# Performance work log

Measured on AMD Instinct MI355X. Metric: run time of the kernel, lower is better.

The kernel has to match this reference:

```python
import jax, jax.numpy as jnp
import numpy as np
import math

TANH_CLIP = 10.0
NEG_INF = -100000000.0

def setup_inputs() -> dict:
    key = jax.random.key(0)
    k1, k2, k3, k4, k5 = jax.random.split(key, 5)
    B, Nq, Nk, D = 64, 1024, 1024, 256
    scale = 1.0 / math.sqrt(D)  # ~xavier-ish scale for weights
    return {
        "q": jax.random.normal(k1, (B, Nq, D), dtype=jnp.float32),
        "k": jax.random.normal(k2, (B, Nk, D), dtype=jnp.float32),
        "w_query": jax.random.normal(k3, (D, D), dtype=jnp.float32) * scale,
        "w_key": jax.random.normal(k4, (D, D), dtype=jnp.float32) * scale,
        "mask": jax.random.randint(k5, (B, Nq, Nk), 0, 2, dtype=jnp.int32),
    }

def reference(q, k, w_query, w_key, mask):
    D = q.shape[-1]
    norm = 1.0 / math.sqrt(D)  # key_dim == embedding_dim
    Q = jnp.einsum("bqd,de->bqe", q, w_query)  # [B,Nq,D]
    K = jnp.einsum("bkd,de->bke", k, w_key)    # [B,Nk,D]
    U = norm * jnp.einsum("bqe,bke->bqk", Q, K)
    U = TANH_CLIP * jnp.tanh(U)
    U = jnp.where(mask == 1, NEG_INF, U)
    return jax.nn.log_softmax(U, axis=-1)
```

## Files before the change

### kernel.cpp

```cpp
#include <hip/hip_runtime.h>
#include <hip/hip_bf16.h>
#include <stdint.h>

#define NEG_INF -100000000.0f

typedef __attribute__((ext_vector_type(8))) short bf16x8;
typedef __attribute__((ext_vector_type(4))) float f32x4;
typedef __attribute__((ext_vector_type(4))) int i32x4;

#define LGKM_BAR()                                                \
    do {                                                          \
        asm volatile("s_waitcnt lgkmcnt(0)" ::: "memory");        \
        __builtin_amdgcn_s_barrier();                             \
        __builtin_amdgcn_sched_barrier(0);                        \
    } while (0)

static __device__ __forceinline__ short f2bf(float x) {
    unsigned u = __float_as_uint(x);
    u = u + 0x7FFFu + ((u >> 16) & 1u);
    return (short)(u >> 16);
}

__global__ void wtrans_kernel(const float* __restrict__ wq, const float* __restrict__ wk,
                              short* __restrict__ wtq, short* __restrict__ wtk) {
    __shared__ float tile[32][33];
    const float* w = blockIdx.z ? wk : wq;
    short* wt = blockIdx.z ? wtk : wtq;
    float scale = blockIdx.z ? 1.0f : 0.0625f;
    int tx = threadIdx.x, ty = threadIdx.y;
    int c0 = blockIdx.x * 32;
    int k0 = blockIdx.y * 32;
#pragma unroll
    for (int i = 0; i < 4; i++)
        tile[ty + i * 8][tx] = w[(k0 + ty + i * 8) * 256 + c0 + tx];
    __syncthreads();
#pragma unroll
    for (int i = 0; i < 4; i++)
        wt[(c0 + ty + i * 8) * 256 + k0 + tx] = f2bf(tile[tx][ty + i * 8] * scale);
}

__global__ __launch_bounds__(512, 4)
void proj_kernel(const float* __restrict__ qin, const float* __restrict__ kin,
                 const short* __restrict__ wtq, const short* __restrict__ wtk,
                 short* __restrict__ Qb, short* __restrict__ Kb,
                 const int* __restrict__ mask, unsigned* __restrict__ pmask) {
    if (blockIdx.y == 2) {
        int t = threadIdx.x;
        size_t row = (size_t)blockIdx.x * 64 + (t >> 3);
        int seg8 = t & 7;
        const int* mrow = mask + row * 1024;
#pragma unroll
        for (int jj = 0; jj < 4; jj++) {
            int j = seg8 + jj * 8;
            unsigned v = 0;
#pragma unroll
            for (int i = 0; i < 8; i++) {
                i32x4 x = __builtin_nontemporal_load(
                    reinterpret_cast<const i32x4*>(mrow + j * 4 + i * 128));
                unsigned nib = (unsigned)(x.x | (x.y << 1) | (x.z << 2) | (x.w << 3));
                v |= nib << (i * 4);
            }
            pmask[row * 32 + j] = v;
        }
        return;
    }

    const float* x  = blockIdx.y ? kin : qin;
    const short* wt = blockIdx.y ? wtk : wtq;
    short* outp     = blockIdx.y ? Kb  : Qb;

    __shared__ __align__(16) short sbuf[64 * 296];
    short* xlds = sbuf;
    short* wlds = sbuf + 2048;

    int t = threadIdx.x;
    int lane = t & 63, w = t >> 6;
    int l15 = lane & 15, g = lane >> 4;
    int rowbase = blockIdx.x * 64;

    f32x4 zero = {0.f, 0.f, 0.f, 0.f};
    f32x4 acc[4][2];
#pragma unroll
    for (int m = 0; m < 4; m++)
#pragma unroll
        for (int n = 0; n < 2; n++) acc[m][n] = zero;

    for (int dc = 0; dc < 8; dc++) {
        __syncthreads();
        {
            int row = t >> 3, seg = t & 7;
            f32x4 v = __builtin_nontemporal_load(
                reinterpret_cast<const f32x4*>(x + (size_t)(rowbase + row) * 256 + dc * 32 + seg * 4));
            short4 bb;
            bb.x = f2bf(v.x); bb.y = f2bf(v.y); bb.z = f2bf(v.z); bb.w = f2bf(v.w);
            *reinterpret_cast<short4*>(&xlds[row * 32 + seg * 4]) = bb;
        }
#pragma unroll
        for (int i = 0; i < 2; i++) {
            int idx = i * 512 + t;
            int c = idx >> 2, seg = idx & 3;
            int4 v = *reinterpret_cast<const int4*>(wt + c * 256 + dc * 32 + seg * 8);
            *reinterpret_cast<int4*>(&wlds[idx * 8]) = v;
        }
        __syncthreads();

        bf16x8 a[4], bfr[2];
#pragma unroll
        for (int m = 0; m < 4; m++)
            a[m] = *reinterpret_cast<const bf16x8*>(&xlds[(m * 16 + l15) * 32 + g * 8]);
#pragma unroll
        for (int n = 0; n < 2; n++) {
            int c = w * 32 + n * 16 + l15;
            bfr[n] = *reinterpret_cast<const bf16x8*>(&wlds[c * 32 + g * 8]);
        }
#pragma unroll
        for (int m = 0; m < 4; m++)
#pragma unroll
            for (int n = 0; n < 2; n++)
                acc[m][n] = __builtin_amdgcn_mfma_f32_16x16x32_bf16(a[m], bfr[n], acc[m][n], 0, 0, 0);
    }

    __syncthreads();
#pragma unroll
    for (int m = 0; m < 4; m++)
#pragma unroll
        for (int n = 0; n < 2; n++) {
            int col = w * 32 + n * 16 + l15;
#pragma unroll
            for (int r = 0; r < 4; r++)
                sbuf[(m * 16 + g * 4 + r) * 296 + col] = f2bf(acc[m][n][r]);
        }
    __syncthreads();

    int b8 = rowbase >> 10;
    int rloc = rowbase & 1023;
#pragma unroll
    for (int o = 0; o < 4; o++) {
        int gu = o * 512 + t;
        int dc = gu >> 8;
        int rem = gu & 255;
        int row = rem >> 2, kseg = rem & 3;
        int4 v = *reinterpret_cast<const int4*>(&sbuf[row * 296 + dc * 32 + kseg * 8]);
        size_t idx = (((size_t)b8 * 8 + dc) * 1024 + rloc + row) * 32 + kseg * 8;
        *reinterpret_cast<int4*>(outp + idx) = v;
    }
}

__global__ __launch_bounds__(512, 4)
void attn_kernel(const short* __restrict__ Qs, const short* __restrict__ Ks,
                 const unsigned* __restrict__ pmask, float* __restrict__ out) {
    const int RS = 1028;
    __shared__ __align__(16) float ulds[16 * RS];

    int t = threadIdx.x;
    int lane = t & 63, w = t >> 6;
    int l15 = lane & 15, g = lane >> 4;

    int bid = blockIdx.x;
    int wg = (bid & 7) * 256 + (bid >> 3);
    int b = wg >> 5;
    int brow = (wg & 31) * 32;

    const unsigned* pm = pmask + ((size_t)b * 1024 + brow) * 32;
    unsigned mbits0 = pm[t];
    unsigned mbits1 = pm[512 + t];

    const short* qb = Qs + (size_t)b * 8 * 1024 * 32;
    const short* kb = Ks + (size_t)b * 8 * 1024 * 32;

    f32x4 zero = {0.f, 0.f, 0.f, 0.f};
    f32x4 acc[2][8];
#pragma unroll
    for (int m = 0; m < 2; m++)
#pragma unroll
        for (int n = 0; n < 8; n++) acc[m][n] = zero;

    for (int dc = 0; dc < 8; dc++) {
        const short* qc = qb + (size_t)dc * 1024 * 32;
        const short* kc = kb + (size_t)dc * 1024 * 32;
        bf16x8 a0 = *reinterpret_cast<const bf16x8*>(qc + (brow + l15) * 32 + g * 8);
        bf16x8 a1 = *reinterpret_cast<const bf16x8*>(qc + (brow + 16 + l15) * 32 + g * 8);
#pragma unroll
        for (int n = 0; n < 8; n++) {
            bf16x8 bf = *reinterpret_cast<const bf16x8*>(kc + (w * 128 + n * 16 + l15) * 32 + g * 8);
            acc[0][n] = __builtin_amdgcn_mfma_f32_16x16x32_bf16(a0, bf, acc[0][n], 0, 0, 0);
            acc[1][n] = __builtin_amdgcn_mfma_f32_16x16x32_bf16(a1, bf, acc[1][n], 0, 0, 0);
        }
    }

    int row = t >> 5;
    int j = t & 31;
    float* urow = ulds + row * RS;

#pragma unroll
    for (int m = 0; m < 2; m++) {
        LGKM_BAR();
#pragma unroll
        for (int n = 0; n < 8; n++)
#pragma unroll
            for (int r = 0; r < 4; r++)
                ulds[(g * 4 + r) * RS + w * 128 + n * 16 + l15] = acc[m][n][r];
        LGKM_BAR();

        unsigned bits = m ? mbits1 : mbits0;

        float psum = 0.f;
#pragma unroll
        for (int i = 0; i < 8; i++) {
            int col = j * 4 + i * 128;
            float4 u4 = *reinterpret_cast<const float4*>(urow + col);
            float uv[4] = {u4.x, u4.y, u4.z, u4.w};
            float uc[4];
#pragma unroll
            for (int c = 0; c < 4; c++) {
                float e2 = __expf(2.0f * uv[c]);
                float tc = 10.0f - 20.0f / (e2 + 1.0f);
                bool msk = (bits >> (i * 4 + c)) & 1;
                uc[c] = msk ? NEG_INF : tc;
                psum += msk ? 0.0f : __expf(tc);
            }
            float4 s = {uc[0], uc[1], uc[2], uc[3]};
            *reinterpret_cast<float4*>(urow + col) = s;
        }
        psum += __shfl_xor(psum, 1);
        psum += __shfl_xor(psum, 2);
        psum += __shfl_xor(psum, 4);
        psum += __shfl_xor(psum, 8);
        psum += __shfl_xor(psum, 16);
        float lse = __logf(fmaxf(psum, 1e-30f));
        float lse0 = __shfl(lse, 0);
        float lse1 = __shfl(lse, 32);

        float* obase = out + ((size_t)b * 1024 + brow + m * 16) * 1024;
#pragma unroll
        for (int rr = 0; rr < 2; rr++) {
            int r2 = w * 2 + rr;
            float lser = rr ? lse1 : lse0;
            const float* ur2 = ulds + r2 * RS;
            float* orow = obase + (size_t)r2 * 1024;
#pragma unroll
            for (int i2 = 0; i2 < 4; i2++) {
                int col = lane * 4 + i2 * 256;
                float4 u4 = *reinterpret_cast<const float4*>(ur2 + col);
                f32x4 o = {u4.x - lser, u4.y - lser, u4.z - lser, u4.w - lser};
                __builtin_nontemporal_store(o, reinterpret_cast<f32x4*>(orow + col));
            }
        }
    }
}

extern "C" void kernel_launch(void* const* d_in, const int* in_sizes, int n_in,
                              void* d_out, int out_size, void* d_ws, size_t ws_size,
                              hipStream_t stream) {
    const float* q  = (const float*)d_in[0];
    const float* k  = (const float*)d_in[1];
    const float* wq = (const float*)d_in[2];
    const float* wk = (const float*)d_in[3];
    const int* mask = (const int*)d_in[4];
    float* out = (float*)d_out;

    char* ws = (char*)d_ws;
    short* wtq = (short*)ws;
    short* wtk = (short*)(ws + 131072);
    short* Qb  = (short*)(ws + 262144);
    short* Kb  = (short*)(ws + 262144 + 33554432);
    unsigned* pmask = (unsigned*)(ws + 262144 + 2 * 33554432);

    wtrans_kernel<<<dim3(8, 8, 2), dim3(32, 8), 0, stream>>>(wq, wk, wtq, wtk);
    proj_kernel<<<dim3(1024, 3), 512, 0, stream>>>(q, k, wtq, wtk, Qb, Kb, mask, pmask);
    attn_kernel<<<dim3(2048), 512, 0, stream>>>(Qb, Kb, pmask, out);
}
```

Measured before the change: 213.1 us.

## Stage K tiles in LDS via direct global-to-LDS loads with 64-row blocks

The attention kernel now uses 1024-thread blocks covering 64 query rows. Each K chunk is loaded once into LDS through global_load_lds, so two row groups of waves share it instead of each wave reading K from global memory. The projection kernel writes K in a swizzled, segment-major layout to match the LDS read pattern and avoid bank conflicts. In exchange the kernel pays more barriers per d-chunk and has fewer, larger blocks, which may lower occupancy.

```diff
diff --git a/kernel.cpp b/kernel.cpp
--- a/kernel.cpp
+++ b/kernel.cpp
@@ -14,6 +14,18 @@
         __builtin_amdgcn_s_barrier();                             \
         __builtin_amdgcn_sched_barrier(0);                        \
     } while (0)
+
+#define VM_BAR()                                                  \
+    do {                                                          \
+        asm volatile("s_waitcnt vmcnt(0)" ::: "memory");          \
+        __builtin_amdgcn_s_barrier();                             \
+        __builtin_amdgcn_sched_barrier(0);                        \
+    } while (0)
+
+#define GLOAD_LDS16(gp, lp)                                                      \
+    __builtin_amdgcn_global_load_lds(                                            \
+        (const __attribute__((address_space(1))) void*)(gp),                     \
+        (__attribute__((address_space(3))) void*)(lp), 16, 0, 0)
 
 static __device__ __forceinline__ short f2bf(float x) {
     unsigned u = __float_as_uint(x);
@@ -134,39 +146,55 @@
 
     int b8 = rowbase >> 10;
     int rloc = rowbase & 1023;
-#pragma unroll
-    for (int o = 0; o < 4; o++) {
-        int gu = o * 512 + t;
-        int dc = gu >> 8;
-        int rem = gu & 255;
-        int row = rem >> 2, kseg = rem & 3;
-        int4 v = *reinterpret_cast<const int4*>(&sbuf[row * 296 + dc * 32 + kseg * 8]);
-        size_t idx = (((size_t)b8 * 8 + dc) * 1024 + rloc + row) * 32 + kseg * 8;
-        *reinterpret_cast<int4*>(outp + idx) = v;
-    }
-}
-
-__global__ __launch_bounds__(512, 4)
+    if (blockIdx.y == 1) {
+#pragma unroll
+        for (int o = 0; o < 4; o++) {
+            int u = o * 512 + t;
+            int dc = u >> 8, s = (u >> 6) & 3, cl = u & 63;
+            int gg = s ^ (cl & 3);
+            int4 v = *reinterpret_cast<const int4*>(&sbuf[cl * 296 + dc * 32 + gg * 8]);
+            size_t idx = (((size_t)b8 * 8 + dc) * 4 + s) * 8192 + (size_t)(rloc + cl) * 8;
+            *reinterpret_cast<int4*>(outp + idx) = v;
+        }
+    } else {
+#pragma unroll
+        for (int o = 0; o < 4; o++) {
+            int gu = o * 512 + t;
+            int dc = gu >> 8;
+            int rem = gu & 255;
+            int row = rem >> 2, kseg = rem & 3;
+            int4 v = *reinterpret_cast<const int4*>(&sbuf[row * 296 + dc * 32 + kseg * 8]);
+            size_t idx = (((size_t)b8 * 8 + dc) * 1024 + rloc + row) * 32 + kseg * 8;
+            *reinterpret_cast<int4*>(outp + idx) = v;
+        }
+    }
+}
+
+__global__ __launch_bounds__(1024, 4)
 void attn_kernel(const short* __restrict__ Qs, const short* __restrict__ Ks,
                  const unsigned* __restrict__ pmask, float* __restrict__ out) {
     const int RS = 1028;
-    __shared__ __align__(16) float ulds[16 * RS];
+    __shared__ __align__(16) char slds[32 * RS * 4];
+
+    char* kldsb = slds;
+    float* plds = (float*)slds;
 
     int t = threadIdx.x;
-    int lane = t & 63, w = t >> 6;
+    int lane = t & 63, wv = t >> 6;
     int l15 = lane & 15, g = lane >> 4;
+    int rowg = wv >> 3, colg = wv & 7;
 
     int bid = blockIdx.x;
-    int wg = (bid & 7) * 256 + (bid >> 3);
-    int b = wg >> 5;
-    int brow = (wg & 31) * 32;
+    int wg = (bid & 7) * 128 + (bid >> 3);
+    int b = wg >> 4;
+    int brow = (wg & 15) * 64;
 
     const unsigned* pm = pmask + ((size_t)b * 1024 + brow) * 32;
-    unsigned mbits0 = pm[t];
-    unsigned mbits1 = pm[512 + t];
-
-    const short* qb = Qs + (size_t)b * 8 * 1024 * 32;
-    const short* kb = Ks + (size_t)b * 8 * 1024 * 32;
+    unsigned mw0 = pm[t];
+    unsigned mw1 = pm[1024 + t];
+
+    const short* qb = Qs + (size_t)b * 8 * 32768;
+    const char* kbb = (const char*)(Ks + (size_t)b * 8 * 32768);
 
     f32x4 zero = {0.f, 0.f, 0.f, 0.f};
     f32x4 acc[2][8];
@@ -175,35 +203,48 @@
 #pragma unroll
         for (int n = 0; n < 8; n++) acc[m][n] = zero;
 
+    int kfoff = ((g ^ (l15 & 3)) << 14) + (colg * 128 + l15) * 16;
+
     for (int dc = 0; dc < 8; dc++) {
-        const short* qc = qb + (size_t)dc * 1024 * 32;
-        const short* kc = kb + (size_t)dc * 1024 * 32;
-        bf16x8 a0 = *reinterpret_cast<const bf16x8*>(qc + (brow + l15) * 32 + g * 8);
-        bf16x8 a1 = *reinterpret_cast<const bf16x8*>(qc + (brow + 16 + l15) * 32 + g * 8);
+        LGKM_BAR();
+        const char* kcb = kbb + dc * 65536;
+        int soff = wv << 12;
+#pragma unroll
+        for (int i = 0; i < 4; i++) {
+            int boff = soff + (i << 10);
+            GLOAD_LDS16(kcb + boff + lane * 16, kldsb + boff);
+        }
+        const short* qc = qb + dc * 32768;
+        bf16x8 a0 = *reinterpret_cast<const bf16x8*>(qc + (brow + rowg * 32 + l15) * 32 + g * 8);
+        bf16x8 a1 = *reinterpret_cast<const bf16x8*>(qc + (brow + rowg * 32 + 16 + l15) * 32 + g * 8);
+        VM_BAR();
 #pragma unroll
         for (int n = 0; n < 8; n++) {
-            bf16x8 bf = *reinterpret_cast<const bf16x8*>(kc + (w * 128 + n * 16 + l15) * 32 + g * 8);
+            bf16x8 bf = *reinterpret_cast<const bf16x8*>(kldsb + kfoff + n * 256);
             acc[0][n] = __builtin_amdgcn_mfma_f32_16x16x32_bf16(a0, bf, acc[0][n], 0, 0, 0);
             acc[1][n] = __builtin_amdgcn_mfma_f32_16x16x32_bf16(a1, bf, acc[1][n], 0, 0, 0);
         }
     }
 
-    int row = t >> 5;
+    int prow = t >> 5;
     int j = t & 31;
-    float* urow = ulds + row * RS;
-
-#pragma unroll
-    for (int m = 0; m < 2; m++) {
+    float* urow = plds + prow * RS;
+
+#pragma unroll
+    for (int p = 0; p < 2; p++) {
         LGKM_BAR();
-#pragma unroll
-        for (int n = 0; n < 8; n++)
-#pragma unroll
-            for (int r = 0; r < 4; r++)
-                ulds[(g * 4 + r) * RS + w * 128 + n * 16 + l15] = acc[m][n][r];
+        if (rowg == p) {
+#pragma unroll
+            for (int m = 0; m < 2; m++)
+#pragma unroll
+                for (int n = 0; n < 8; n++)
+#pragma unroll
+                    for (int r = 0; r < 4; r++)
+                        plds[(m * 16 + g * 4 + r) * RS + colg * 128 + n * 16 + l15] = acc[m][n][r];
+        }
         LGKM_BAR();
 
-        unsigned bits = m ? mbits1 : mbits0;
-
+        unsigned bits = p ? mw1 : mw0;
         float psum = 0.f;
 #pragma unroll
         for (int i = 0; i < 8; i++) {
@@ -231,12 +272,12 @@
         float lse0 = __shfl(lse, 0);
         float lse1 = __shfl(lse, 32);
 
-        float* obase = out + ((size_t)b * 1024 + brow + m * 16) * 1024;
+        float* obase = out + ((size_t)b * 1024 + brow + p * 32) * 1024;
 #pragma unroll
         for (int rr = 0; rr < 2; rr++) {
-            int r2 = w * 2 + rr;
+            int r2 = wv * 2 + rr;
             float lser = rr ? lse1 : lse0;
-            const float* ur2 = ulds + r2 * RS;
+            const float* ur2 = plds + r2 * RS;
             float* orow = obase + (size_t)r2 * 1024;
 #pragma unroll
             for (int i2 = 0; i2 < 4; i2++) {
@@ -268,5 +309,5 @@
 
     wtrans_kernel<<<dim3(8, 8, 2), dim3(32, 8), 0, stream>>>(wq, wk, wtq, wtk);
     proj_kernel<<<dim3(1024, 3), 512, 0, stream>>>(q, k, wtq, wtk, Qb, Kb, mask, pmask);
-    attn_kernel<<<dim3(2048), 512, 0, stream>>>(Qb, Kb, pmask, out);
-}
+    attn_kernel<<<dim3(1024), 1024, 0, stream>>>(Qb, Kb, pmask, out);
+}
```

Result: slower. 227.9 us (+7.0%).

## Split fused attention into QK^T kernel with bf16 U and separate softmax epilogue

Applied to the files above, without the earlier changes.

The fused attention kernel is split in two. A QK^T kernel writes the raw scores as bf16 to a workspace buffer, and a separate epilogue kernel applies tanh clipping, the mask and log-softmax, with one wave per row. The mask packing order changes to contiguous bits to match the new epilogue indexing. The aim is to relieve LDS and register pressure in the fused kernel, but it adds a full bf16 round trip of U through memory and rounds the scores to bf16 before the tanh.

```diff
diff --git a/kernel.cpp b/kernel.cpp
--- a/kernel.cpp
+++ b/kernel.cpp
@@ -7,6 +7,7 @@
 typedef __attribute__((ext_vector_type(8))) short bf16x8;
 typedef __attribute__((ext_vector_type(4))) float f32x4;
 typedef __attribute__((ext_vector_type(4))) int i32x4;
+typedef __attribute__((ext_vector_type(2))) int i32x2;
 
 #define LGKM_BAR()                                                \
     do {                                                          \
@@ -19,6 +20,9 @@
     unsigned u = __float_as_uint(x);
     u = u + 0x7FFFu + ((u >> 16) & 1u);
     return (short)(u >> 16);
+}
+static __device__ __forceinline__ float bf2f(short s) {
+    return __uint_as_float(((unsigned)(unsigned short)s) << 16);
 }
 
 __global__ void wtrans_kernel(const float* __restrict__ wq, const float* __restrict__ wk,
@@ -56,9 +60,9 @@
 #pragma unroll
             for (int i = 0; i < 8; i++) {
                 i32x4 x = __builtin_nontemporal_load(
-                    reinterpret_cast<const i32x4*>(mrow + j * 4 + i * 128));
-                unsigned nib = (unsigned)(x.x | (x.y << 1) | (x.z << 2) | (x.w << 3));
-                v |= nib << (i * 4);
+                    reinterpret_cast<const i32x4*>(mrow + j * 32 + i * 4));
+                v |= ((unsigned)x.x << (i * 4)) | ((unsigned)x.y << (i * 4 + 1)) |
+                     ((unsigned)x.z << (i * 4 + 2)) | ((unsigned)x.w << (i * 4 + 3));
             }
             pmask[row * 32 + j] = v;
         }
@@ -147,10 +151,10 @@
 }
 
 __global__ __launch_bounds__(512, 4)
-void attn_kernel(const short* __restrict__ Qs, const short* __restrict__ Ks,
-                 const unsigned* __restrict__ pmask, float* __restrict__ out) {
-    const int RS = 1028;
-    __shared__ __align__(16) float ulds[16 * RS];
+void qkt_kernel(const short* __restrict__ Qs, const short* __restrict__ Ks,
+                short* __restrict__ U) {
+    const int RS = 1042;
+    __shared__ __align__(16) short ulds[16 * RS];
 
     int t = threadIdx.x;
     int lane = t & 63, w = t >> 6;
@@ -161,12 +165,8 @@
     int b = wg >> 5;
     int brow = (wg & 31) * 32;
 
-    const unsigned* pm = pmask + ((size_t)b * 1024 + brow) * 32;
-    unsigned mbits0 = pm[t];
-    unsigned mbits1 = pm[512 + t];
-
-    const short* qb = Qs + (size_t)b * 8 * 1024 * 32;
-    const short* kb = Ks + (size_t)b * 8 * 1024 * 32;
+    const short* qb = Qs + (size_t)b * 8 * 32768;
+    const short* kb = Ks + (size_t)b * 8 * 32768;
 
     f32x4 zero = {0.f, 0.f, 0.f, 0.f};
     f32x4 acc[2][8];
@@ -176,8 +176,8 @@
         for (int n = 0; n < 8; n++) acc[m][n] = zero;
 
     for (int dc = 0; dc < 8; dc++) {
-        const short* qc = qb + (size_t)dc * 1024 * 32;
-        const short* kc = kb + (size_t)dc * 1024 * 32;
+        const short* qc = qb + dc * 32768;
+        const short* kc = kb + dc * 32768;
         bf16x8 a0 = *reinterpret_cast<const bf16x8*>(qc + (brow + l15) * 32 + g * 8);
         bf16x8 a1 = *reinterpret_cast<const bf16x8*>(qc + (brow + 16 + l15) * 32 + g * 8);
 #pragma unroll
@@ -188,10 +188,6 @@
         }
     }
 
-    int row = t >> 5;
-    int j = t & 31;
-    float* urow = ulds + row * RS;
-
 #pragma unroll
     for (int m = 0; m < 2; m++) {
         LGKM_BAR();
@@ -199,53 +195,67 @@
         for (int n = 0; n < 8; n++)
 #pragma unroll
             for (int r = 0; r < 4; r++)
-                ulds[(g * 4 + r) * RS + w * 128 + n * 16 + l15] = acc[m][n][r];
+                ulds[(g * 4 + r) * RS + w * 128 + n * 16 + l15] = f2bf(acc[m][n][r]);
         LGKM_BAR();
 
-        unsigned bits = m ? mbits1 : mbits0;
-
-        float psum = 0.f;
-#pragma unroll
-        for (int i = 0; i < 8; i++) {
-            int col = j * 4 + i * 128;
-            float4 u4 = *reinterpret_cast<const float4*>(urow + col);
-            float uv[4] = {u4.x, u4.y, u4.z, u4.w};
-            float uc[4];
-#pragma unroll
-            for (int c = 0; c < 4; c++) {
-                float e2 = __expf(2.0f * uv[c]);
-                float tc = 10.0f - 20.0f / (e2 + 1.0f);
-                bool msk = (bits >> (i * 4 + c)) & 1;
-                uc[c] = msk ? NEG_INF : tc;
-                psum += msk ? 0.0f : __expf(tc);
-            }
-            float4 s = {uc[0], uc[1], uc[2], uc[3]};
-            *reinterpret_cast<float4*>(urow + col) = s;
-        }
-        psum += __shfl_xor(psum, 1);
-        psum += __shfl_xor(psum, 2);
-        psum += __shfl_xor(psum, 4);
-        psum += __shfl_xor(psum, 8);
-        psum += __shfl_xor(psum, 16);
-        float lse = __logf(fmaxf(psum, 1e-30f));
-        float lse0 = __shfl(lse, 0);
-        float lse1 = __shfl(lse, 32);
-
-        float* obase = out + ((size_t)b * 1024 + brow + m * 16) * 1024;
+        short* ubase = U + ((size_t)b * 1024 + brow + m * 16) * 1024;
 #pragma unroll
         for (int rr = 0; rr < 2; rr++) {
             int r2 = w * 2 + rr;
-            float lser = rr ? lse1 : lse0;
-            const float* ur2 = ulds + r2 * RS;
-            float* orow = obase + (size_t)r2 * 1024;
-#pragma unroll
-            for (int i2 = 0; i2 < 4; i2++) {
-                int col = lane * 4 + i2 * 256;
-                float4 u4 = *reinterpret_cast<const float4*>(ur2 + col);
-                f32x4 o = {u4.x - lser, u4.y - lser, u4.z - lser, u4.w - lser};
-                __builtin_nontemporal_store(o, reinterpret_cast<f32x4*>(orow + col));
+            short* urow = ubase + (size_t)r2 * 1024;
+#pragma unroll
+            for (int it = 0; it < 2; it++) {
+                int col = lane * 8 + it * 512;
+                i32x4 v = *reinterpret_cast<const i32x4*>(&ulds[r2 * RS + col]);
+                __builtin_nontemporal_store(v, reinterpret_cast<i32x4*>(urow + col));
             }
         }
+    }
+}
+
+__global__ __launch_bounds__(256)
+void epi_kernel(const short* __restrict__ U, const unsigned* __restrict__ pmask,
+                float* __restrict__ out) {
+    int t = threadIdx.x;
+    int lane = t & 63, wv = t >> 6;
+    size_t row = (size_t)blockIdx.x * 4 + wv;
+
+    const short* urow = U + row * 1024;
+    const unsigned* pmrow = pmask + row * 32;
+
+    float uc[4][4];
+    float psum = 0.f;
+#pragma unroll
+    for (int it = 0; it < 4; it++) {
+        int c0 = lane * 4 + it * 256;
+        i32x2 raw = __builtin_nontemporal_load(reinterpret_cast<const i32x2*>(urow + c0));
+        unsigned bits = (pmrow[c0 >> 5] >> (c0 & 31)) & 0xF;
+        short s4[4] = {(short)(raw.x & 0xFFFF), (short)(raw.x >> 16),
+                       (short)(raw.y & 0xFFFF), (short)(raw.y >> 16)};
+#pragma unroll
+        for (int c = 0; c < 4; c++) {
+            float u = bf2f(s4[c]);
+            float e2 = __expf(2.0f * u);
+            float tc = 10.0f - 20.0f / (e2 + 1.0f);
+            bool msk = (bits >> c) & 1;
+            uc[it][c] = msk ? NEG_INF : tc;
+            psum += msk ? 0.0f : __expf(tc);
+        }
+    }
+    psum += __shfl_xor(psum, 1);
+    psum += __shfl_xor(psum, 2);
+    psum += __shfl_xor(psum, 4);
+    psum += __shfl_xor(psum, 8);
+    psum += __shfl_xor(psum, 16);
+    psum += __shfl_xor(psum, 32);
+    float lse = __logf(fmaxf(psum, 1e-30f));
+
+    float* orow = out + row * 1024;
+#pragma unroll
+    for (int it = 0; it < 4; it++) {
+        int c0 = lane * 4 + it * 256;
+        f32x4 o = {uc[it][0] - lse, uc[it][1] - lse, uc[it][2] - lse, uc[it][3] - lse};
+        __builtin_nontemporal_store(o, reinterpret_cast<f32x4*>(orow + c0));
     }
 }
 
@@ -265,8 +275,10 @@
     short* Qb  = (short*)(ws + 262144);
     short* Kb  = (short*)(ws + 262144 + 33554432);
     unsigned* pmask = (unsigned*)(ws + 262144 + 2 * 33554432);
+    short* U = (short*)(ws + 262144 + 2 * 33554432 + 8388608);
 
     wtrans_kernel<<<dim3(8, 8, 2), dim3(32, 8), 0, stream>>>(wq, wk, wtq, wtk);
     proj_kernel<<<dim3(1024, 3), 512, 0, stream>>>(q, k, wtq, wtk, Qb, Kb, mask, pmask);
-    attn_kernel<<<dim3(2048), 512, 0, stream>>>(Qb, Kb, pmask, out);
-}
+    qkt_kernel<<<dim3(2048), 512, 0, stream>>>(Qb, Kb, U);
+    epi_kernel<<<dim3(16384), 256, 0, stream>>>(U, pmask, out);
+}
```

Result: slower. 377.0 us (+76.9%).

## Double-buffer projection LDS tiles and store attention scores as bf16 in LDS

Applied to the files above, without the earlier changes.

The projection kernel now double-buffers the x and weight tiles in shared memory. It prefetches the next chunk into registers while the MFMAs run on the current one, which drops one barrier per iteration. The attention kernel stores the logits as bf16 in two separate LDS buffers, so both 16-row halves are staged up front and the post-processing needs fewer barriers. This halves LDS traffic for the score tile. The cost is that clipped logits are rounded to bf16 before the log-softmax subtraction, which lowers output precision.

```diff
diff --git a/kernel.cpp b/kernel.cpp
--- a/kernel.cpp
+++ b/kernel.cpp
@@ -69,15 +69,22 @@
     const short* wt = blockIdx.y ? wtk : wtq;
     short* outp     = blockIdx.y ? Kb  : Qb;
 
-    __shared__ __align__(16) short sbuf[64 * 296];
-    short* xlds = sbuf;
-    short* wlds = sbuf + 2048;
+    __shared__ __align__(16) char slds[40960];
+    short* xl0 = (short*)slds;
+    short* wl0 = xl0 + 2048;
+    short* xl1 = (short*)(slds + 20480);
+    short* wl1 = xl1 + 2048;
 
     int t = threadIdx.x;
     int lane = t & 63, w = t >> 6;
     int l15 = lane & 15, g = lane >> 4;
     int rowbase = blockIdx.x * 64;
 
+    int srow = t >> 3, sseg = t & 7;
+    const float* xrow = x + (size_t)(rowbase + srow) * 256 + sseg * 4;
+    int wc0 = t >> 2, wseg0 = t & 3;
+    int wc1 = (512 + t) >> 2, wseg1 = t & 3;
+
     f32x4 zero = {0.f, 0.f, 0.f, 0.f};
     f32x4 acc[4][2];
 #pragma unroll
@@ -85,42 +92,57 @@
 #pragma unroll
         for (int n = 0; n < 2; n++) acc[m][n] = zero;
 
+    {
+        f32x4 xv = __builtin_nontemporal_load(reinterpret_cast<const f32x4*>(xrow));
+        int4 wv0 = *reinterpret_cast<const int4*>(wt + wc0 * 256 + wseg0 * 8);
+        int4 wv1 = *reinterpret_cast<const int4*>(wt + wc1 * 256 + wseg1 * 8);
+        short4 bb; bb.x = f2bf(xv.x); bb.y = f2bf(xv.y); bb.z = f2bf(xv.z); bb.w = f2bf(xv.w);
+        *reinterpret_cast<short4*>(&xl0[srow * 32 + sseg * 4]) = bb;
+        *reinterpret_cast<int4*>(&wl0[(size_t)t * 8]) = wv0;
+        *reinterpret_cast<int4*>(&wl0[((size_t)512 + t) * 8]) = wv1;
+    }
+    LGKM_BAR();
+
+#pragma unroll
     for (int dc = 0; dc < 8; dc++) {
-        __syncthreads();
-        {
-            int row = t >> 3, seg = t & 7;
-            f32x4 v = __builtin_nontemporal_load(
-                reinterpret_cast<const f32x4*>(x + (size_t)(rowbase + row) * 256 + dc * 32 + seg * 4));
-            short4 bb;
-            bb.x = f2bf(v.x); bb.y = f2bf(v.y); bb.z = f2bf(v.z); bb.w = f2bf(v.w);
-            *reinterpret_cast<short4*>(&xlds[row * 32 + seg * 4]) = bb;
-        }
-#pragma unroll
-        for (int i = 0; i < 2; i++) {
-            int idx = i * 512 + t;
-            int c = idx >> 2, seg = idx & 3;
-            int4 v = *reinterpret_cast<const int4*>(wt + c * 256 + dc * 32 + seg * 8);
-            *reinterpret_cast<int4*>(&wlds[idx * 8]) = v;
-        }
-        __syncthreads();
+        short* xc   = (dc & 1) ? xl1 : xl0;
+        short* wcur = (dc & 1) ? wl1 : wl0;
+        short* xn   = (dc & 1) ? xl0 : xl1;
+        short* wn   = (dc & 1) ? wl0 : wl1;
+
+        f32x4 xv; int4 wv0, wv1;
+        if (dc < 7) {
+            xv  = __builtin_nontemporal_load(reinterpret_cast<const f32x4*>(xrow + (dc + 1) * 32));
+            wv0 = *reinterpret_cast<const int4*>(wt + wc0 * 256 + (dc + 1) * 32 + wseg0 * 8);
+            wv1 = *reinterpret_cast<const int4*>(wt + wc1 * 256 + (dc + 1) * 32 + wseg1 * 8);
+        }
 
         bf16x8 a[4], bfr[2];
 #pragma unroll
         for (int m = 0; m < 4; m++)
-            a[m] = *reinterpret_cast<const bf16x8*>(&xlds[(m * 16 + l15) * 32 + g * 8]);
+            a[m] = *reinterpret_cast<const bf16x8*>(&xc[(m * 16 + l15) * 32 + g * 8]);
 #pragma unroll
         for (int n = 0; n < 2; n++) {
             int c = w * 32 + n * 16 + l15;
-            bfr[n] = *reinterpret_cast<const bf16x8*>(&wlds[c * 32 + g * 8]);
+            bfr[n] = *reinterpret_cast<const bf16x8*>(&wcur[c * 32 + g * 8]);
         }
 #pragma unroll
         for (int m = 0; m < 4; m++)
 #pragma unroll
             for (int n = 0; n < 2; n++)
                 acc[m][n] = __builtin_amdgcn_mfma_f32_16x16x32_bf16(a[m], bfr[n], acc[m][n], 0, 0, 0);
-    }
-
-    __syncthreads();
+
+        if (dc < 7) {
+            short4 bb; bb.x = f2bf(xv.x); bb.y = f2bf(xv.y); bb.z = f2bf(xv.z); bb.w = f2bf(xv.w);
+            *reinterpret_cast<short4*>(&xn[srow * 32 + sseg * 4]) = bb;
+            *reinterpret_cast<int4*>(&wn[(size_t)t * 8]) = wv0;
+            *reinterpret_cast<int4*>(&wn[((size_t)512 + t) * 8]) = wv1;
+            LGKM_BAR();
+        }
+    }
+
+    LGKM_BAR();
+    short* sdump = (short*)slds;
 #pragma unroll
     for (int m = 0; m < 4; m++)
 #pragma unroll
@@ -128,9 +150,9 @@
             int col = w * 32 + n * 16 + l15;
 #pragma unroll
             for (int r = 0; r < 4; r++)
-                sbuf[(m * 16 + g * 4 + r) * 296 + col] = f2bf(acc[m][n][r]);
-        }
-    __syncthreads();
+                sdump[(m * 16 + g * 4 + r) * 296 + col] = f2bf(acc[m][n][r]);
+        }
+    LGKM_BAR();
 
     int b8 = rowbase >> 10;
     int rloc = rowbase & 1023;
@@ -140,7 +162,7 @@
         int dc = gu >> 8;
         int rem = gu & 255;
         int row = rem >> 2, kseg = rem & 3;
-        int4 v = *reinterpret_cast<const int4*>(&sbuf[row * 296 + dc * 32 + kseg * 8]);
+        int4 v = *reinterpret_cast<const int4*>(&sdump[row * 296 + dc * 32 + kseg * 8]);
         size_t idx = (((size_t)b8 * 8 + dc) * 1024 + rloc + row) * 32 + kseg * 8;
         *reinterpret_cast<int4*>(outp + idx) = v;
     }
@@ -149,8 +171,9 @@
 __global__ __launch_bounds__(512, 4)
 void attn_kernel(const short* __restrict__ Qs, const short* __restrict__ Ks,
                  const unsigned* __restrict__ pmask, float* __restrict__ out) {
-    const int RS = 1028;
-    __shared__ __align__(16) float ulds[16 * RS];
+    const int RSB = 1034;
+    __shared__ __align__(16) short ulds0[16 * RSB];
+    __shared__ __align__(16) short ulds1[16 * RSB];
 
     int t = threadIdx.x;
     int lane = t & 63, w = t >> 6;
@@ -162,11 +185,11 @@
     int brow = (wg & 31) * 32;
 
     const unsigned* pm = pmask + ((size_t)b * 1024 + brow) * 32;
-    unsigned mbits0 = pm[t];
-    unsigned mbits1 = pm[512 + t];
-
-    const short* qb = Qs + (size_t)b * 8 * 1024 * 32;
-    const short* kb = Ks + (size_t)b * 8 * 1024 * 32;
+    unsigned mw0 = pm[t];
+    unsigned mw1 = pm[512 + t];
+
+    const short* qb = Qs + (size_t)b * 8 * 32768;
+    const short* kb = Ks + (size_t)b * 8 * 32768;
 
     f32x4 zero = {0.f, 0.f, 0.f, 0.f};
     f32x4 acc[2][8];
@@ -176,8 +199,8 @@
         for (int n = 0; n < 8; n++) acc[m][n] = zero;
 
     for (int dc = 0; dc < 8; dc++) {
-        const short* qc = qb + (size_t)dc * 1024 * 32;
-        const short* kc = kb + (size_t)dc * 1024 * 32;
+        const short* qc = qb + dc * 32768;
+        const short* kc = kb + dc * 32768;
         bf16x8 a0 = *reinterpret_cast<const bf16x8*>(qc + (brow + l15) * 32 + g * 8);
         bf16x8 a1 = *reinterpret_cast<const bf16x8*>(qc + (brow + 16 + l15) * 32 + g * 8);
 #pragma unroll
@@ -188,39 +211,48 @@
         }
     }
 
-    int row = t >> 5;
+    int prow = t >> 5;
     int j = t & 31;
-    float* urow = ulds + row * RS;
+
+#pragma unroll
+    for (int n = 0; n < 8; n++)
+#pragma unroll
+        for (int r = 0; r < 4; r++)
+            ulds0[(g * 4 + r) * RSB + w * 128 + n * 16 + l15] = f2bf(acc[0][n][r]);
+    LGKM_BAR();
+
+#pragma unroll
+    for (int n = 0; n < 8; n++)
+#pragma unroll
+        for (int r = 0; r < 4; r++)
+            ulds1[(g * 4 + r) * RSB + w * 128 + n * 16 + l15] = f2bf(acc[1][n][r]);
 
 #pragma unroll
     for (int m = 0; m < 2; m++) {
-        LGKM_BAR();
-#pragma unroll
-        for (int n = 0; n < 8; n++)
-#pragma unroll
-            for (int r = 0; r < 4; r++)
-                ulds[(g * 4 + r) * RS + w * 128 + n * 16 + l15] = acc[m][n][r];
-        LGKM_BAR();
-
-        unsigned bits = m ? mbits1 : mbits0;
+        short* buf = m ? ulds1 : ulds0;
+        unsigned bits = m ? mw1 : mw0;
+        short* urow = buf + prow * RSB;
 
         float psum = 0.f;
 #pragma unroll
         for (int i = 0; i < 8; i++) {
             int col = j * 4 + i * 128;
-            float4 u4 = *reinterpret_cast<const float4*>(urow + col);
-            float uv[4] = {u4.x, u4.y, u4.z, u4.w};
-            float uc[4];
+            unsigned lo = *reinterpret_cast<const unsigned*>(&urow[col]);
+            unsigned hi = *reinterpret_cast<const unsigned*>(&urow[col + 2]);
+            float uv[4] = {__uint_as_float(lo << 16), __uint_as_float(lo & 0xffff0000u),
+                           __uint_as_float(hi << 16), __uint_as_float(hi & 0xffff0000u)};
+            unsigned short ucb[4];
 #pragma unroll
             for (int c = 0; c < 4; c++) {
                 float e2 = __expf(2.0f * uv[c]);
                 float tc = 10.0f - 20.0f / (e2 + 1.0f);
                 bool msk = (bits >> (i * 4 + c)) & 1;
-                uc[c] = msk ? NEG_INF : tc;
+                float uc = msk ? NEG_INF : tc;
+                ucb[c] = (unsigned short)f2bf(uc);
                 psum += msk ? 0.0f : __expf(tc);
             }
-            float4 s = {uc[0], uc[1], uc[2], uc[3]};
-            *reinterpret_cast<float4*>(urow + col) = s;
+            *reinterpret_cast<unsigned*>(&urow[col]) = (unsigned)ucb[0] | ((unsigned)ucb[1] << 16);
+            *reinterpret_cast<unsigned*>(&urow[col + 2]) = (unsigned)ucb[2] | ((unsigned)ucb[3] << 16);
         }
         psum += __shfl_xor(psum, 1);
         psum += __shfl_xor(psum, 2);
@@ -236,16 +268,21 @@
         for (int rr = 0; rr < 2; rr++) {
             int r2 = w * 2 + rr;
             float lser = rr ? lse1 : lse0;
-            const float* ur2 = ulds + r2 * RS;
+            const short* ur2 = buf + r2 * RSB;
             float* orow = obase + (size_t)r2 * 1024;
 #pragma unroll
             for (int i2 = 0; i2 < 4; i2++) {
                 int col = lane * 4 + i2 * 256;
-                float4 u4 = *reinterpret_cast<const float4*>(ur2 + col);
-                f32x4 o = {u4.x - lser, u4.y - lser, u4.z - lser, u4.w - lser};
+                unsigned lo = *reinterpret_cast<const unsigned*>(&ur2[col]);
+                unsigned hi = *reinterpret_cast<const unsigned*>(&ur2[col + 2]);
+                f32x4 o = {__uint_as_float(lo << 16) - lser,
+                           __uint_as_float(lo & 0xffff0000u) - lser,
+                           __uint_as_float(hi << 16) - lser,
+                           __uint_as_float(hi & 0xffff0000u) - lser};
                 __builtin_nontemporal_store(o, reinterpret_cast<f32x4*>(orow + col));
             }
         }
+        if (m == 0) LGKM_BAR();
     }
 }
 
```

New measurement: 215.5 us. About the same (+1.1%).
